# Kernel tuning notes

Measured on AMD Instinct MI355X. Metric: run time of the kernel, lower is better.

The kernel has to match this reference:

```python
import jax, jax.numpy as jnp
import numpy as np

DIM = 1024
NUM_HEADS = 16
HEAD_DIM = DIM // NUM_HEADS


def _slopes(num_heads):
    ratio = 2.0 ** (-8.0 / num_heads)
    return jnp.asarray([ratio ** i for i in range(1, num_heads + 1)], dtype=jnp.float32)


def setup_inputs() -> dict:
    key = jax.random.key(0)
    ks = jax.random.split(key, 10)
    b, q_len, k_len = 2, 2048, 4096
    query = jax.random.normal(ks[0], (b, q_len, DIM), dtype=jnp.float32)
    keys = jax.random.normal(ks[1], (b, k_len, DIM), dtype=jnp.float32)
    values = jax.random.normal(ks[2], (b, k_len, DIM), dtype=jnp.float32)
    query_pos = jnp.sort(jax.random.randint(ks[3], (b, q_len), 0, 8192), axis=-1)
    key_pos = jnp.sort(jax.random.randint(ks[4], (b, k_len), 0, 8192), axis=-1)
    mask = jnp.ones((b, q_len, k_len), dtype=jnp.int32)
    # xavier-uniform-like linear weights, torch layout [out, in]
    lim = float(np.sqrt(6.0 / (DIM + DIM)))
    W_q = jax.random.uniform(ks[5], (DIM, DIM), minval=-lim, maxval=lim, dtype=jnp.float32)
    W_k = jax.random.uniform(ks[6], (DIM, DIM), minval=-lim, maxval=lim, dtype=jnp.float32)
    W_v = jax.random.uniform(ks[7], (DIM, DIM), minval=-lim, maxval=lim, dtype=jnp.float32)
    W_o = jax.random.uniform(ks[8], (DIM, DIM), minval=-lim, maxval=lim, dtype=jnp.float32)
    return {"query": query, "keys": keys, "values": values,
            "W_q": W_q, "W_k": W_k, "W_v": W_v, "W_o": W_o,
            "query_pos": query_pos, "key_pos": key_pos, "mask": mask}


def reference(query, keys, values, W_q, W_k, W_v, W_o, query_pos, key_pos, mask):
    b, q_len, _ = query.shape
    k_len = keys.shape[1]
    scale = 1.0 / np.sqrt(HEAD_DIM)
    # project and split heads: [b, h, len, d]
    Q = (query @ W_q.T).reshape(b, q_len, NUM_HEADS, HEAD_DIM).transpose(0, 2, 1, 3)
    K = (keys @ W_k.T).reshape(b, k_len, NUM_HEADS, HEAD_DIM).transpose(0, 2, 1, 3)
    V = (values @ W_v.T).reshape(b, k_len, NUM_HEADS, HEAD_DIM).transpose(0, 2, 1, 3)
    scores = jnp.einsum('bhqd,bhkd->bhqk', Q, K) * scale
    # ALiBi bias: -slope_h * (q_pos - k_pos)
    dist = (query_pos[:, :, None] - key_pos[:, None, :]).astype(scores.dtype)  # [b,q,k]
    bias = -_slopes(NUM_HEADS)[None, :, None, None] * dist[:, None, :, :]
    scores = scores + bias
    scores = jnp.where(mask[:, None, :, :] == 0, -jnp.inf, scores)
    # softmax1 exactly as source: exp(x - max) / (1 + sum(exp(x - max)))
    m = jnp.max(scores, axis=-1, keepdims=True)
    e = jnp.exp(scores - m)
    attn = e / (1.0 + jnp.sum(e, axis=-1, keepdims=True))
    out = jnp.einsum('bhqk,bhkd->bhqd', attn, V)
    out = out.transpose(0, 2, 1, 3).reshape(b, q_len, DIM)
    return out @ W_o.T
```

## Files before the change

kernel.cpp:

```cpp
#include <hip/hip_runtime.h>


typedef short bf16x8 __attribute__((ext_vector_type(8)));
typedef short s16x4  __attribute__((ext_vector_type(4)));
typedef float f32x4  __attribute__((ext_vector_type(4)));

#define MFMA16(a,b,c) __builtin_amdgcn_mfma_f32_16x16x32_bf16(a,b,c,0,0,0)

__device__ __forceinline__ short f2bf(float x) {
  unsigned u = __float_as_uint(x);
  u = (u + 0x7fffu + ((u >> 16) & 1u)) >> 16;
  return (short)u;
}

__device__ __forceinline__ unsigned cvt_pk_bf16(float a, float b) {
  unsigned r;
  asm("v_cvt_pk_bf16_f32 %0, %1, %2" : "=v"(r) : "v"(a), "v"(b));
  return r;
}

__device__ __forceinline__ void gload16(const void* g, void* l) {
  __builtin_amdgcn_global_load_lds((const __attribute__((address_space(1))) void*)g,
                                   (__attribute__((address_space(3))) void*)l, 16, 0, 0);
}

__global__ __launch_bounds__(256) void convert_kernel(
    const float* __restrict__ q,  const float* __restrict__ k,  const float* __restrict__ v,
    const float* __restrict__ wq, const float* __restrict__ wk, const float* __restrict__ wv,
    const float* __restrict__ wo,
    short* __restrict__ qb, short* __restrict__ kb, short* __restrict__ vb,
    short* __restrict__ wqb, short* __restrict__ wkb, short* __restrict__ wvb,
    short* __restrict__ wob)
{
  long c = (long)blockIdx.x * 256 + threadIdx.x;
  const float QSCALE = 0.125f * 1.44269504088896f;
  const float* src; short* dst; long base; float scale = 1.0f;
  if      (c < 1048576) { src = q;  dst = qb;  base = 0;       }
  else if (c < 3145728) { src = k;  dst = kb;  base = 1048576; }
  else if (c < 5242880) { src = v;  dst = vb;  base = 3145728; }
  else if (c < 5505024) { src = wq; dst = wqb; base = 5242880; scale = QSCALE; }
  else if (c < 5767168) { src = wk; dst = wkb; base = 5505024; }
  else if (c < 6029312) { src = wv; dst = wvb; base = 5767168; }
  else                  { src = wo; dst = wob; base = 6029312; }
  long i = (c - base) * 4;
  float4 x = *(const float4*)(src + i);
  s16x4 o = { f2bf(x.x * scale), f2bf(x.y * scale), f2bf(x.z * scale), f2bf(x.w * scale) };
  *(s16x4*)(dst + i) = o;
}

template<int MODE, int BM>
__global__ __launch_bounds__(256) void gemm_bt(const short* __restrict__ A,
                                               const short* __restrict__ B,
                                               void* __restrict__ Cout)
{
  constexpr int WCOLS = (BM == 128) ? 2 : 4;
  constexpr int TN    = 128 / WCOLS;
  constexpr int NI    = TN / 16;
  constexpr int APASS = BM / 32;
  __shared__ alignas(16) short As[2][BM * 64];
  __shared__ alignas(16) short Bs[2][128 * 64];
  const int tid  = threadIdx.x;
  const int wave = tid >> 6, lane = tid & 63;
  const int lo = lane & 15, g = lane >> 4;
  const int wm = wave / WCOLS, wn = wave % WCOLS;
  const int m0 = blockIdx.x * BM, n0 = blockIdx.y * 128;

  f32x4 acc[4][NI];
  const f32x4 Z4 = {0.f, 0.f, 0.f, 0.f};
#pragma unroll
  for (int i = 0; i < 4; i++)
#pragma unroll
    for (int j = 0; j < NI; j++) acc[i][j] = Z4;

  auto stage = [&](int buf, int k0) {
#pragma unroll
    for (int i = 0; i < APASS; i++) {
      int c = i * 256 + tid;
      gload16(A + (long)(m0 + (c >> 3)) * 1024 + k0 + (c & 7) * 8,
              &As[buf][(i * 256 + wave * 64) * 8]);
    }
#pragma unroll
    for (int i = 0; i < 4; i++) {
      int c = i * 256 + tid;
      gload16(B + (long)(n0 + (c >> 3)) * 1024 + k0 + (c & 7) * 8,
              &Bs[buf][(i * 256 + wave * 64) * 8]);
    }
  };

  stage(0, 0);
  __syncthreads();
  int cur = 0;
  for (int t = 0; t < 16; t++) {
    if (t < 15) stage(cur ^ 1, (t + 1) * 64);
#pragma unroll
    for (int kk = 0; kk < 2; kk++) {
      bf16x8 af[4], bfr[NI];
#pragma unroll
      for (int mi = 0; mi < 4; mi++)
        af[mi] = *(const bf16x8*)&As[cur][(wm * 64 + mi * 16 + lo) * 64 + kk * 32 + g * 8];
#pragma unroll
      for (int ni = 0; ni < NI; ni++)
        bfr[ni] = *(const bf16x8*)&Bs[cur][(wn * TN + ni * 16 + lo) * 64 + kk * 32 + g * 8];
#pragma unroll
      for (int mi = 0; mi < 4; mi++)
#pragma unroll
        for (int ni = 0; ni < NI; ni++)
          acc[mi][ni] = MFMA16(af[mi], bfr[ni], acc[mi][ni]);
    }
    __syncthreads();
    cur ^= 1;
  }

  const int rbase = m0 + wm * 64, cbase = n0 + wn * TN;
  if (MODE == 0 || MODE == 2) {
#pragma unroll
    for (int mi = 0; mi < 4; mi++)
#pragma unroll
      for (int ni = 0; ni < NI; ni++) {
        int row = rbase + mi * 16 + g * 4;
        int col = cbase + ni * 16 + lo;
#pragma unroll
        for (int r = 0; r < 4; r++) {
          if (MODE == 0) ((short*)Cout)[(long)(row + r) * 1024 + col] = f2bf(acc[mi][ni][r]);
          else           ((float*)Cout)[(long)(row + r) * 1024 + col] = acc[mi][ni][r];
        }
      }
  } else {
#pragma unroll
    for (int mi = 0; mi < 4; mi++)
#pragma unroll
      for (int ni = 0; ni < NI; ni++) {
        int mrow = rbase + mi * 16 + g * 4;
        int n    = cbase + ni * 16 + lo;
        int b    = mrow >> 12, key = mrow & 4095;
        s16x4 pk = { f2bf(acc[mi][ni][0]), f2bf(acc[mi][ni][1]),
                     f2bf(acc[mi][ni][2]), f2bf(acc[mi][ni][3]) };
        *(s16x4*)((short*)Cout + ((long)(b * 1024 + n)) * 4096 + key) = pk;
      }
  }
}

#define ATTN_BODY(KC, KN, KB, PREF)                                              \
  {                                                                              \
    if (PREF) {                                                                  \
      _Pragma("unroll") for (int nk = 0; nk < 4; nk++)                           \
      _Pragma("unroll") for (int kk = 0; kk < 2; kk++)                           \
        KN[kk][nk] = *(const bf16x8*)(Kl + (long)((KB) + 64 + 4 * (nk & 1)       \
                                      + 32 * (nk >> 1)) * 1024 + kk * 32);       \
    }                                                                            \
    bf16x8 vf[2][4];                                                             \
    _Pragma("unroll") for (int k2 = 0; k2 < 2; k2++)                             \
    _Pragma("unroll") for (int ni = 0; ni < 4; ni++)                             \
      vf[k2][ni] = *(const bf16x8*)(Vl[ni] + (KB) + k2 * 32);                    \
    float4 sk[4];                                                                \
    _Pragma("unroll") for (int nk = 0; nk < 4; nk++)                             \
      sk[nk] = *(const float4*)&skp_lds[(KB) + 8 * g + 4 * (nk & 1)              \
                                        + 32 * (nk >> 1)];                       \
    _Pragma("unroll") for (int grp = 0; grp < 2; grp++) {                        \
      f32x4 S[4];                                                                \
      _Pragma("unroll") for (int nk = 0; nk < 4; nk++) S[nk] = Z4;               \
      __builtin_amdgcn_s_setprio(1);                                             \
      _Pragma("unroll") for (int nk = 0; nk < 4; nk++)                           \
      _Pragma("unroll") for (int kk = 0; kk < 2; kk++)                           \
        S[nk] = MFMA16(KC[kk][nk], qf[grp][kk], S[nk]);                          \
      __builtin_amdgcn_s_setprio(0);                                             \
      _Pragma("unroll") for (int nk = 0; nk < 4; nk++)                           \
      _Pragma("unroll") for (int r = 0; r < 4; r++) S[nk][r] += sk[nk][r];       \
      float rm = fmaxf(                                                          \
        fmaxf(fmaxf(fmaxf(S[0][0],S[0][1]), fmaxf(S[0][2],S[0][3])),             \
              fmaxf(fmaxf(S[1][0],S[1][1]), fmaxf(S[1][2],S[1][3]))),            \
        fmaxf(fmaxf(fmaxf(S[2][0],S[2][1]), fmaxf(S[2][2],S[2][3])),             \
              fmaxf(fmaxf(S[3][0],S[3][1]), fmaxf(S[3][2],S[3][3]))));           \
      rm = fmaxf(rm, __shfl_xor(rm, 16));                                        \
      rm = fmaxf(rm, __shfl_xor(rm, 32));                                        \
      float mn2 = fmaxf(m_[grp], rm);                                            \
      float rfac = exp2f(m_[grp] - mn2);                                         \
      m_[grp] = mn2;                                                             \
      float p[4][4];                                                             \
      _Pragma("unroll") for (int nk = 0; nk < 4; nk++)                           \
      _Pragma("unroll") for (int r = 0; r < 4; r++)                              \
        p[nk][r] = exp2f(S[nk][r] - mn2);                                        \
      float rs = ((p[0][0]+p[0][1]) + (p[0][2]+p[0][3]))                         \
               + ((p[1][0]+p[1][1]) + (p[1][2]+p[1][3]))                         \
               + ((p[2][0]+p[2][1]) + (p[2][2]+p[2][3]))                         \
               + ((p[3][0]+p[3][1]) + (p[3][2]+p[3][3]));                        \
      rs += __shfl_xor(rs, 16);                                                  \
      rs += __shfl_xor(rs, 32);                                                  \
      l_[grp] = l_[grp] * rfac + rs;                                             \
      union { unsigned u[4]; bf16x8 v; } pb0, pb1;                               \
      pb0.u[0] = cvt_pk_bf16(p[0][0], p[0][1]);                                  \
      pb0.u[1] = cvt_pk_bf16(p[0][2], p[0][3]);                                  \
      pb0.u[2] = cvt_pk_bf16(p[1][0], p[1][1]);                                  \
      pb0.u[3] = cvt_pk_bf16(p[1][2], p[1][3]);                                  \
      pb1.u[0] = cvt_pk_bf16(p[2][0], p[2][1]);                                  \
      pb1.u[1] = cvt_pk_bf16(p[2][2], p[2][3]);                                  \
      pb1.u[2] = cvt_pk_bf16(p[3][0], p[3][1]);                                  \
      pb1.u[3] = cvt_pk_bf16(p[3][2], p[3][3]);                                  \
      _Pragma("unroll") for (int ni = 0; ni < 4; ni++)                           \
      _Pragma("unroll") for (int r = 0; r < 4; r++) acc[grp][ni][r] *= rfac;     \
      __builtin_amdgcn_s_setprio(1);                                             \
      _Pragma("unroll") for (int ni = 0; ni < 4; ni++) {                         \
        acc[grp][ni] = MFMA16(vf[0][ni], pb0.v, acc[grp][ni]);                   \
        acc[grp][ni] = MFMA16(vf[1][ni], pb1.v, acc[grp][ni]);                   \
      }                                                                          \
      __builtin_amdgcn_s_setprio(0);                                             \
    }                                                                            \
  }

__global__ __launch_bounds__(256) void attn_kernel(
    const short* __restrict__ Qp, const short* __restrict__ Kp, const short* __restrict__ Vt,
    const int* __restrict__ kpos, short* __restrict__ AO)
{
  __shared__ float skp_lds[4096];
  const int tid = threadIdx.x;
  const int wv = tid >> 6, lane = tid & 63;
  const int lo = lane & 15, g = lane >> 4;
  const int bh = blockIdx.x, qt = blockIdx.y;
  const int b = bh >> 4, h = bh & 15;
  const float slope2 = exp2f(-0.5f * (float)(h + 1)) * 1.44269504088896f;

  for (int i = tid; i < 4096; i += 256)
    skp_lds[i] = slope2 * (float)kpos[b * 4096 + i];
  __syncthreads();

  const long qrow = (long)b * 2048 + qt * 128 + wv * 32;

  bf16x8 qf[2][2];
#pragma unroll
  for (int grp = 0; grp < 2; grp++)
#pragma unroll
    for (int kk = 0; kk < 2; kk++)
      qf[grp][kk] = *(const bf16x8*)(Qp + (qrow + grp * 16 + lo) * 1024
                                     + h * 64 + kk * 32 + g * 8);

  float m_[2], l_[2];
  f32x4 acc[2][4];
  const f32x4 Z4 = {0.f, 0.f, 0.f, 0.f};
#pragma unroll
  for (int grp = 0; grp < 2; grp++) {
    m_[grp] = -__builtin_inff(); l_[grp] = 0.f;
#pragma unroll
    for (int ni = 0; ni < 4; ni++) acc[grp][ni] = Z4;
  }

  const short* Kl = Kp + (long)b * 4096 * 1024 + h * 64
                    + (long)(8 * (lo >> 2) + (lo & 3)) * 1024 + g * 8;
  const short* Vl[4];
#pragma unroll
  for (int ni = 0; ni < 4; ni++)
    Vl[ni] = Vt + (long)bh * 64 * 4096 + (long)(ni * 16 + lo) * 4096 + g * 8;

  bf16x8 kfa[2][4], kfb[2][4];
#pragma unroll
  for (int nk = 0; nk < 4; nk++)
#pragma unroll
    for (int kk = 0; kk < 2; kk++)
      kfa[kk][nk] = *(const bf16x8*)(Kl + (long)(4 * (nk & 1) + 32 * (nk >> 1)) * 1024
                                     + kk * 32);

  int kb = 0;
  for (int it = 0; it < 31; it++, kb += 128) {
    ATTN_BODY(kfa, kfb, kb,      true)
    ATTN_BODY(kfb, kfa, kb + 64, true)
  }
  ATTN_BODY(kfa, kfb, 3968, true)
  ATTN_BODY(kfb, kfa, 4032, false)

#pragma unroll
  for (int grp = 0; grp < 2; grp++) {
    float inv = 1.0f / (1.0f + l_[grp]);
    long rowq = qrow + grp * 16 + lo;
#pragma unroll
    for (int ni = 0; ni < 4; ni++) {
      uint2 w = { cvt_pk_bf16(acc[grp][ni][0] * inv, acc[grp][ni][1] * inv),
                  cvt_pk_bf16(acc[grp][ni][2] * inv, acc[grp][ni][3] * inv) };
      *(uint2*)(AO + rowq * 1024 + h * 64 + ni * 16 + g * 4) = w;
    }
  }
}

extern "C" void kernel_launch(void* const* d_in, const int* in_sizes, int n_in,
                              void* d_out, int out_size, void* d_ws, size_t ws_size,
                              hipStream_t stream)
{
  const float* q  = (const float*)d_in[0];
  const float* k  = (const float*)d_in[1];
  const float* v  = (const float*)d_in[2];
  const float* wq = (const float*)d_in[3];
  const float* wk = (const float*)d_in[4];
  const float* wv = (const float*)d_in[5];
  const float* wo = (const float*)d_in[6];
  const int* kpos = (const int*)d_in[8];

  char* ws = (char*)d_ws;
  const size_t MB = 1u << 20;
  short* qbf = (short*)(ws + 0  * MB);
  short* kbf = (short*)(ws + 8  * MB);
  short* vbf = (short*)(ws + 24 * MB);
  short* wqb = (short*)(ws + 40 * MB);
  short* wkb = (short*)(ws + 42 * MB);
  short* wvb = (short*)(ws + 44 * MB);
  short* wob = (short*)(ws + 46 * MB);
  short* Qp  = (short*)(ws + 48 * MB);
  short* Kp  = (short*)(ws + 56 * MB);
  short* Vt  = (short*)(ws + 72 * MB);
  short* AO  = (short*)(ws + 88 * MB);

  convert_kernel<<<24576, 256, 0, stream>>>(q, k, v, wq, wk, wv, wo,
                                            qbf, kbf, vbf, wqb, wkb, wvb, wob);
  gemm_bt<0, 64> <<<dim3(64, 8), 256, 0, stream>>>(qbf, wqb, Qp);
  gemm_bt<0, 128><<<dim3(64, 8), 256, 0, stream>>>(kbf, wkb, Kp);
  gemm_bt<1, 128><<<dim3(64, 8), 256, 0, stream>>>(vbf, wvb, Vt);
  attn_kernel<<<dim3(32, 16), 256, 0, stream>>>(Qp, Kp, Vt, kpos, AO);
  gemm_bt<2, 64> <<<dim3(64, 8), 256, 0, stream>>>(AO, wob, d_out);
}
```

Baseline: 513.0 us.

## Split attention over key halves with combine kernel and fuse QKV projections

Attention now runs with two key-range splits per query tile, doubling the grid. Each split writes unnormalized fp32 partial outputs plus running max and sum, and a new combine kernel merges them and applies the softmax1 normalization. The three input projection GEMMs are fused into one launch that dispatches on block index. This targets low occupancy in the attention kernel and launch overhead, at the cost of extra fp32 partial traffic and another kernel launch.

Result: slower. 533.0 us (+3.9%).

```diff
diff --git a/kernel.cpp b/kernel.cpp
--- a/kernel.cpp
+++ b/kernel.cpp
@@ -48,33 +48,34 @@
   *(s16x4*)(dst + i) = o;
 }
 
-template<int MODE, int BM>
-__global__ __launch_bounds__(256) void gemm_bt(const short* __restrict__ A,
-                                               const short* __restrict__ B,
-                                               void* __restrict__ Cout)
-{
-  constexpr int WCOLS = (BM == 128) ? 2 : 4;
-  constexpr int TN    = 128 / WCOLS;
-  constexpr int NI    = TN / 16;
-  constexpr int APASS = BM / 32;
-  __shared__ alignas(16) short As[2][BM * 64];
+__global__ __launch_bounds__(256) void proj_kernel(
+    const short* __restrict__ A,
+    const short* __restrict__ wqb, const short* __restrict__ wkb, const short* __restrict__ wvb,
+    short* __restrict__ Qp, short* __restrict__ Kp, short* __restrict__ Vt)
+{
+  __shared__ alignas(16) short As[2][128 * 64];
   __shared__ alignas(16) short Bs[2][128 * 64];
+  const int bx = blockIdx.x;
+  const short* B; short* outp; int outbase; bool vmode;
+  if (bx < 32)      { B = wqb; outp = Qp; outbase = 0;     vmode = false; }
+  else if (bx < 96) { B = wkb; outp = Kp; outbase = 4096;  vmode = false; }
+  else              { B = wvb; outp = Vt; outbase = 12288; vmode = true;  }
   const int tid  = threadIdx.x;
   const int wave = tid >> 6, lane = tid & 63;
   const int lo = lane & 15, g = lane >> 4;
-  const int wm = wave / WCOLS, wn = wave % WCOLS;
-  const int m0 = blockIdx.x * BM, n0 = blockIdx.y * 128;
-
-  f32x4 acc[4][NI];
+  const int wm = wave >> 1, wn = wave & 1;
+  const int m0 = bx * 128, n0 = blockIdx.y * 128;
+
+  f32x4 acc[4][4];
   const f32x4 Z4 = {0.f, 0.f, 0.f, 0.f};
 #pragma unroll
   for (int i = 0; i < 4; i++)
 #pragma unroll
-    for (int j = 0; j < NI; j++) acc[i][j] = Z4;
+    for (int j = 0; j < 4; j++) acc[i][j] = Z4;
 
   auto stage = [&](int buf, int k0) {
 #pragma unroll
-    for (int i = 0; i < APASS; i++) {
+    for (int i = 0; i < 4; i++) {
       int c = i * 256 + tid;
       gload16(A + (long)(m0 + (c >> 3)) * 1024 + k0 + (c & 7) * 8,
               &As[buf][(i * 256 + wave * 64) * 8]);
@@ -94,50 +95,115 @@
     if (t < 15) stage(cur ^ 1, (t + 1) * 64);
 #pragma unroll
     for (int kk = 0; kk < 2; kk++) {
-      bf16x8 af[4], bfr[NI];
+      bf16x8 af[4], bfr[4];
 #pragma unroll
       for (int mi = 0; mi < 4; mi++)
         af[mi] = *(const bf16x8*)&As[cur][(wm * 64 + mi * 16 + lo) * 64 + kk * 32 + g * 8];
 #pragma unroll
-      for (int ni = 0; ni < NI; ni++)
-        bfr[ni] = *(const bf16x8*)&Bs[cur][(wn * TN + ni * 16 + lo) * 64 + kk * 32 + g * 8];
+      for (int ni = 0; ni < 4; ni++)
+        bfr[ni] = *(const bf16x8*)&Bs[cur][(wn * 64 + ni * 16 + lo) * 64 + kk * 32 + g * 8];
 #pragma unroll
       for (int mi = 0; mi < 4; mi++)
 #pragma unroll
-        for (int ni = 0; ni < NI; ni++)
+        for (int ni = 0; ni < 4; ni++)
           acc[mi][ni] = MFMA16(af[mi], bfr[ni], acc[mi][ni]);
     }
     __syncthreads();
     cur ^= 1;
   }
 
-  const int rbase = m0 + wm * 64, cbase = n0 + wn * TN;
-  if (MODE == 0 || MODE == 2) {
+  const int rbase = m0 - outbase + wm * 64, cbase = n0 + wn * 64;
+  if (!vmode) {
 #pragma unroll
     for (int mi = 0; mi < 4; mi++)
 #pragma unroll
-      for (int ni = 0; ni < NI; ni++) {
+      for (int ni = 0; ni < 4; ni++) {
         int row = rbase + mi * 16 + g * 4;
         int col = cbase + ni * 16 + lo;
 #pragma unroll
-        for (int r = 0; r < 4; r++) {
-          if (MODE == 0) ((short*)Cout)[(long)(row + r) * 1024 + col] = f2bf(acc[mi][ni][r]);
-          else           ((float*)Cout)[(long)(row + r) * 1024 + col] = acc[mi][ni][r];
-        }
+        for (int r = 0; r < 4; r++)
+          outp[(long)(row + r) * 1024 + col] = f2bf(acc[mi][ni][r]);
       }
   } else {
 #pragma unroll
     for (int mi = 0; mi < 4; mi++)
 #pragma unroll
-      for (int ni = 0; ni < NI; ni++) {
-        int mrow = rbase + mi * 16 + g * 4;
+      for (int ni = 0; ni < 4; ni++) {
+        int vrow = rbase + mi * 16 + g * 4;
         int n    = cbase + ni * 16 + lo;
-        int b    = mrow >> 12, key = mrow & 4095;
+        int b    = vrow >> 12, key = vrow & 4095;
         s16x4 pk = { f2bf(acc[mi][ni][0]), f2bf(acc[mi][ni][1]),
                      f2bf(acc[mi][ni][2]), f2bf(acc[mi][ni][3]) };
-        *(s16x4*)((short*)Cout + ((long)(b * 1024 + n)) * 4096 + key) = pk;
+        *(s16x4*)(outp + ((long)(b * 1024 + n)) * 4096 + key) = pk;
       }
   }
+}
+
+__global__ __launch_bounds__(256) void oproj_kernel(const short* __restrict__ A,
+                                                    const short* __restrict__ B,
+                                                    float* __restrict__ Cout)
+{
+  __shared__ alignas(16) short As[2][64 * 64];
+  __shared__ alignas(16) short Bs[2][128 * 64];
+  const int tid  = threadIdx.x;
+  const int wave = tid >> 6, lane = tid & 63;
+  const int lo = lane & 15, g = lane >> 4;
+  const int m0 = blockIdx.x * 64, n0 = blockIdx.y * 128;
+
+  f32x4 acc[4][2];
+  const f32x4 Z4 = {0.f, 0.f, 0.f, 0.f};
+#pragma unroll
+  for (int i = 0; i < 4; i++) { acc[i][0] = Z4; acc[i][1] = Z4; }
+
+  auto stage = [&](int buf, int k0) {
+#pragma unroll
+    for (int i = 0; i < 2; i++) {
+      int c = i * 256 + tid;
+      gload16(A + (long)(m0 + (c >> 3)) * 1024 + k0 + (c & 7) * 8,
+              &As[buf][(i * 256 + wave * 64) * 8]);
+    }
+#pragma unroll
+    for (int i = 0; i < 4; i++) {
+      int c = i * 256 + tid;
+      gload16(B + (long)(n0 + (c >> 3)) * 1024 + k0 + (c & 7) * 8,
+              &Bs[buf][(i * 256 + wave * 64) * 8]);
+    }
+  };
+
+  stage(0, 0);
+  __syncthreads();
+  int cur = 0;
+  for (int t = 0; t < 16; t++) {
+    if (t < 15) stage(cur ^ 1, (t + 1) * 64);
+#pragma unroll
+    for (int kk = 0; kk < 2; kk++) {
+      bf16x8 af[4], bfr[2];
+#pragma unroll
+      for (int mi = 0; mi < 4; mi++)
+        af[mi] = *(const bf16x8*)&As[cur][(mi * 16 + lo) * 64 + kk * 32 + g * 8];
+#pragma unroll
+      for (int ni = 0; ni < 2; ni++)
+        bfr[ni] = *(const bf16x8*)&Bs[cur][(wave * 32 + ni * 16 + lo) * 64 + kk * 32 + g * 8];
+#pragma unroll
+      for (int mi = 0; mi < 4; mi++)
+#pragma unroll
+        for (int ni = 0; ni < 2; ni++)
+          acc[mi][ni] = MFMA16(af[mi], bfr[ni], acc[mi][ni]);
+    }
+    __syncthreads();
+    cur ^= 1;
+  }
+
+#pragma unroll
+  for (int mi = 0; mi < 4; mi++)
+#pragma unroll
+    for (int ni = 0; ni < 2; ni++) {
+      int row = m0 + mi * 16 + g * 4;
+      int col = n0 + wave * 32 + ni * 16 + lo;
+#pragma unroll
+      for (int r = 0; r < 4; r++)
+        Cout[(long)(row + r) * 1024 + col] = acc[mi][ni][r];
+    }
 }
 
 #define ATTN_BODY(KC, KN, KB, PREF)                                              \
@@ -154,7 +220,7 @@
       vf[k2][ni] = *(const bf16x8*)(Vl[ni] + (KB) + k2 * 32);                    \
     float4 sk[4];                                                                \
     _Pragma("unroll") for (int nk = 0; nk < 4; nk++)                             \
-      sk[nk] = *(const float4*)&skp_lds[(KB) + 8 * g + 4 * (nk & 1)              \
+      sk[nk] = *(const float4*)&skp_lds[(KB) - kb0 + 8 * g + 4 * (nk & 1)        \
                                         + 32 * (nk >> 1)];                       \
     _Pragma("unroll") for (int grp = 0; grp < 2; grp++) {                        \
       f32x4 S[4];                                                                \
@@ -209,18 +275,19 @@
 
 __global__ __launch_bounds__(256) void attn_kernel(
     const short* __restrict__ Qp, const short* __restrict__ Kp, const short* __restrict__ Vt,
-    const int* __restrict__ kpos, short* __restrict__ AO)
-{
-  __shared__ float skp_lds[4096];
+    const int* __restrict__ kpos, float* __restrict__ Opart, float* __restrict__ mlpart)
+{
+  __shared__ float skp_lds[2048];
   const int tid = threadIdx.x;
   const int wv = tid >> 6, lane = tid & 63;
   const int lo = lane & 15, g = lane >> 4;
-  const int bh = blockIdx.x, qt = blockIdx.y;
+  const int bh = blockIdx.x, qt = blockIdx.y, split = blockIdx.z;
   const int b = bh >> 4, h = bh & 15;
+  const int kb0 = split * 2048;
   const float slope2 = exp2f(-0.5f * (float)(h + 1)) * 1.44269504088896f;
 
-  for (int i = tid; i < 4096; i += 256)
-    skp_lds[i] = slope2 * (float)kpos[b * 4096 + i];
+  for (int i = tid; i < 2048; i += 256)
+    skp_lds[i] = slope2 * (float)kpos[b * 4096 + kb0 + i];
   __syncthreads();
 
   const long qrow = (long)b * 2048 + qt * 128 + wv * 32;
@@ -255,27 +322,62 @@
   for (int nk = 0; nk < 4; nk++)
 #pragma unroll
     for (int kk = 0; kk < 2; kk++)
-      kfa[kk][nk] = *(const bf16x8*)(Kl + (long)(4 * (nk & 1) + 32 * (nk >> 1)) * 1024
+      kfa[kk][nk] = *(const bf16x8*)(Kl + (long)(kb0 + 4 * (nk & 1) + 32 * (nk >> 1)) * 1024
                                      + kk * 32);
 
-  int kb = 0;
-  for (int it = 0; it < 31; it++, kb += 128) {
-    ATTN_BODY(kfa, kfb, kb,      true)
-    ATTN_BODY(kfb, kfa, kb + 64, true)
-  }
-  ATTN_BODY(kfa, kfb, 3968, true)
-  ATTN_BODY(kfb, kfa, 4032, false)
-
+  int kb = kb0;
+  for (int it = 0; it < 15; it++) {
+    ATTN_BODY(kfa, kfb, kb, true)  kb += 64;
+    ATTN_BODY(kfb, kfa, kb, true)  kb += 64;
+  }
+  ATTN_BODY(kfa, kfb, kb, true)  kb += 64;
+  ATTN_BODY(kfb, kfa, kb, false)
+
+  const long pbase = ((long)(split * 512 + bh * 16 + qt) * 4 + wv) * 2048;
+  const long mbase = ((long)(split * 512 + bh * 16 + qt) * 4 + wv) * 64;
 #pragma unroll
   for (int grp = 0; grp < 2; grp++) {
-    float inv = 1.0f / (1.0f + l_[grp]);
-    long rowq = qrow + grp * 16 + lo;
-#pragma unroll
-    for (int ni = 0; ni < 4; ni++) {
-      uint2 w = { cvt_pk_bf16(acc[grp][ni][0] * inv, acc[grp][ni][1] * inv),
-                  cvt_pk_bf16(acc[grp][ni][2] * inv, acc[grp][ni][3] * inv) };
-      *(uint2*)(AO + rowq * 1024 + h * 64 + ni * 16 + g * 4) = w;
-    }
+#pragma unroll
+    for (int ni = 0; ni < 4; ni++)
+      *(f32x4*)&Opart[pbase + (grp * 16 + lo) * 64 + ni * 16 + g * 4] = acc[grp][ni];
+    if (g == 0) {
+      mlpart[mbase + grp * 16 + lo]      = m_[grp];
+      mlpart[mbase + 32 + grp * 16 + lo] = l_[grp];
+    }
+  }
+}
+
+__global__ __launch_bounds__(256) void combine_kernel(
+    const float* __restrict__ Opart, const float* __restrict__ mlpart,
+    short* __restrict__ AO)
+{
+  const int b0 = blockIdx.x;
+  const int t = threadIdx.x;
+  const int wv = t >> 6, lane = t & 63;
+  const int qidx = lane >> 1, dh = (lane & 1) * 32;
+  const int bh = b0 >> 4, qt = b0 & 15;
+  const int b = bh >> 4, h = bh & 15;
+
+  const long p0 = ((long)(b0) * 4 + wv) * 2048 + qidx * 64 + dh;
+  const long p1 = ((long)(512 + b0) * 4 + wv) * 2048 + qidx * 64 + dh;
+  const long m0i = ((long)(b0) * 4 + wv) * 64 + qidx;
+  const long m1i = ((long)(512 + b0) * 4 + wv) * 64 + qidx;
+  float m1 = mlpart[m0i], l1 = mlpart[m0i + 32];
+  float m2 = mlpart[m1i], l2 = mlpart[m1i + 32];
+  float M = fmaxf(m1, m2);
+  float a1 = exp2f(m1 - M), a2 = exp2f(m2 - M);
+  float inv = 1.0f / (1.0f + l1 * a1 + l2 * a2);
+  a1 *= inv; a2 *= inv;
+
+  const long row = (long)b * 2048 + qt * 128 + wv * 32 + qidx;
+  short* dst = AO + row * 1024 + h * 64 + dh;
+#pragma unroll
+  for (int j = 0; j < 8; j++) {
+    float4 o1 = *(const float4*)&Opart[p0 + j * 4];
+    float4 o2 = *(const float4*)&Opart[p1 + j * 4];
+    uint2 w = { cvt_pk_bf16(o1.x * a1 + o2.x * a2, o1.y * a1 + o2.y * a2),
+                cvt_pk_bf16(o1.z * a1 + o2.z * a2, o1.w * a1 + o2.w * a2) };
+    *(uint2*)(dst + j * 4) = w;
   }
 }
 
@@ -305,12 +407,13 @@
   short* Kp  = (short*)(ws + 56 * MB);
   short* Vt  = (short*)(ws + 72 * MB);
   short* AO  = (short*)(ws + 88 * MB);
+  float* Opart  = (float*)(ws + 0 * MB);
+  float* mlpart = (float*)(ws + 32 * MB);
 
   convert_kernel<<<24576, 256, 0, stream>>>(q, k, v, wq, wk, wv, wo,
                                             qbf, kbf, vbf, wqb, wkb, wvb, wob);
-  gemm_bt<0, 64> <<<dim3(64, 8), 256, 0, stream>>>(qbf, wqb, Qp);
-  gemm_bt<0, 128><<<dim3(64, 8), 256, 0, stream>>>(kbf, wkb, Kp);
-  gemm_bt<1, 128><<<dim3(64, 8), 256, 0, stream>>>(vbf, wvb, Vt);
-  attn_kernel<<<dim3(32, 16), 256, 0, stream>>>(Qp, Kp, Vt, kpos, AO);
-  gemm_bt<2, 64> <<<dim3(64, 8), 256, 0, stream>>>(AO, wob, d_out);
-}
+  proj_kernel<<<dim3(160, 8), 256, 0, stream>>>(qbf, wqb, wkb, wvb, Qp, Kp, Vt);
+  attn_kernel<<<dim3(32, 16, 2), 256, 0, stream>>>(Qp, Kp, Vt, kpos, Opart, mlpart);
+  combine_kernel<<<512, 256, 0, stream>>>(Opart, mlpart, AO);
+  oproj_kernel<<<dim3(64, 8), 256, 0, stream>>>(AO, wob, (float*)d_out);
+}
```
